# Performance work log

Measured on AMD Instinct MI355X. Metric: run time of the kernel, lower is better.

The kernel has to match this reference:

```python
import jax, jax.numpy as jnp
import numpy as np

N_NODES = 50000
N_HYPEREDGES = 50000
E = 320000
D = 256


def _prelu(x, a):
    return jnp.where(x >= 0, x, a * x)


def _hypergraph_conv(x, hei, W, b, num_nodes, num_edges):
    # PyG HypergraphConv, use_attention=False, heads=1:
    # out = D^{-1} H B^{-1} H^T (X W^T) + b
    src = hei[0]  # node indices, [E]
    he = hei[1]   # hyperedge indices, [E]
    xw = x @ W.T  # [N, D] node transform (lin has no bias)
    ones = jnp.ones((hei.shape[1],), x.dtype)
    deg_n = jax.ops.segment_sum(ones, src, num_segments=num_nodes)   # node degree D
    deg_e = jax.ops.segment_sum(ones, he, num_segments=num_edges)    # hyperedge size B
    d_inv = jnp.where(deg_n > 0, 1.0 / deg_n, 0.0)
    b_inv = jnp.where(deg_e > 0, 1.0 / deg_e, 0.0)
    # node -> hyperedge aggregation, scaled by B^{-1}
    edge_feat = b_inv[:, None] * jax.ops.segment_sum(xw[src], he, num_segments=num_edges)  # [n_he, D]
    # hyperedge -> node aggregation, scaled by D^{-1}
    out = d_inv[:, None] * jax.ops.segment_sum(edge_feat[he], src, num_segments=num_nodes)  # [N, D]
    return out + b


def setup_inputs() -> dict:
    key = jax.random.key(0)
    ks = jax.random.split(key, 6)
    std = np.sqrt(2.0 / D)  # kaiming_normal
    x = jax.random.normal(ks[0], (N_NODES, D), dtype=jnp.float32)
    hyper_edge_index = jax.random.randint(ks[1], (2, E), 0, N_HYPEREDGES, dtype=jnp.int64)
    W1 = jax.random.normal(ks[2], (D, D), dtype=jnp.float32) * std
    b1 = jnp.zeros((D,), jnp.float32)
    W2 = jax.random.normal(ks[3], (D, D), dtype=jnp.float32) * std
    b2 = jnp.zeros((D,), jnp.float32)
    prelu_a = jnp.asarray(0.25, jnp.float32)
    return {"x": x, "W1": W1, "b1": b1, "W2": W2, "b2": b2,
            "prelu_a": prelu_a, "hyper_edge_index": hyper_edge_index}


def reference(x, W1, b1, W2, b2, prelu_a, hyper_edge_index):
    out = _hypergraph_conv(x, hyper_edge_index, W1, b1, N_NODES, N_HYPEREDGES)
    out = _prelu(out, prelu_a)
    out = _hypergraph_conv(out, hyper_edge_index, W2, b2, N_NODES, N_HYPEREDGES)
    out = out + x  # residual
    out = _prelu(out, prelu_a)
    return out
```

## Files before the change

### kernel.cpp

```cpp
#include <hip/hip_runtime.h>

#define NN    50000
#define NHE   50000
#define NEDGE 320000
#define DD    256

#define SB    1024
#define NBLK  ((NN + SB - 1) / SB)

typedef float f32x4 __attribute__((ext_vector_type(4)));
typedef short short8 __attribute__((ext_vector_type(8)));

static __device__ __forceinline__ unsigned short f2b(float f) {
    union { float f; unsigned u; } c; c.f = f;
    unsigned u = c.u;
    u += 0x7fffu + ((u >> 16) & 1u);
    return (unsigned short)(u >> 16);
}
static __device__ __forceinline__ float b2f_lo(unsigned v) {
    union { unsigned u; float f; } c; c.u = v << 16; return c.f;
}
static __device__ __forceinline__ float b2f_hi(unsigned v) {
    union { unsigned u; float f; } c; c.u = v & 0xffff0000u; return c.f;
}
static __device__ __forceinline__ unsigned pack2(float a, float b) {
    return (unsigned)f2b(a) | ((unsigned)f2b(b) << 16);
}

__global__ __launch_bounds__(256) void k_count(const int* __restrict__ src,
                                               const int* __restrict__ he,
                                               int* __restrict__ cnt_n,
                                               int* __restrict__ cnt_e) {
    int e = blockIdx.x * 256 + threadIdx.x;
    if (e >= NEDGE) return;
    atomicAdd(&cnt_n[src[e]], 1);
    atomicAdd(&cnt_e[he[e]], 1);
}

__global__ __launch_bounds__(256) void k_scan_a(const int* __restrict__ cnt_n,
                                                const int* __restrict__ cnt_e,
                                                int* __restrict__ bsum) {
    int b   = blockIdx.x;
    int seg = b / NBLK, lb = b % NBLK;
    const int* cnt = seg ? cnt_e : cnt_n;
    int t = threadIdx.x;
    int idx = lb * SB + t * 4;
    int s = 0;
#pragma unroll
    for (int j = 0; j < 4; ++j)
        if (idx + j < NN) s += cnt[idx + j];
    __shared__ int red[256];
    red[t] = s;
    __syncthreads();
    for (int o = 128; o > 0; o >>= 1) {
        if (t < o) red[t] += red[t + o];
        __syncthreads();
    }
    if (t == 0) bsum[b] = red[0];
}

__global__ __launch_bounds__(64) void k_scan_b(const int* __restrict__ bsum,
                                               int* __restrict__ bbase) {
    if (threadIdx.x == 0) {
        int r = 0;
        for (int i = 0; i < NBLK; ++i) { bbase[i] = r; r += bsum[i]; }
        bbase[2 * NBLK] = r;
        r = 0;
        for (int i = NBLK; i < 2 * NBLK; ++i) { bbase[i] = r; r += bsum[i]; }
        bbase[2 * NBLK + 1] = r;
    }
}

__global__ __launch_bounds__(256) void k_scan_c(const int* __restrict__ cnt_n,
                                                const int* __restrict__ cnt_e,
                                                const int* __restrict__ bbase,
                                                int* __restrict__ off_n,
                                                int* __restrict__ off_e) {
    int b   = blockIdx.x;
    int seg = b / NBLK, lb = b % NBLK;
    const int* cnt = seg ? cnt_e : cnt_n;
    int* off = seg ? off_e : off_n;
    int t = threadIdx.x;
    int idx = lb * SB + t * 4;
    int v[4];
    int tsum = 0;
#pragma unroll
    for (int j = 0; j < 4; ++j) {
        v[j] = (idx + j < NN) ? cnt[idx + j] : 0;
        tsum += v[j];
    }
    __shared__ int sc[256];
    sc[t] = tsum;
    __syncthreads();
    for (int o = 1; o < 256; o <<= 1) {
        int val = (t >= o) ? sc[t - o] : 0;
        __syncthreads();
        sc[t] += val;
        __syncthreads();
    }
    int p = bbase[b] + sc[t] - tsum;
#pragma unroll
    for (int j = 0; j < 4; ++j) {
        if (idx + j < NN) off[idx + j] = p;
        p += v[j];
    }
    if (b == 0 && t == 0) off_n[NN] = bbase[2 * NBLK];
    if (b == NBLK && t == 0) off_e[NHE] = bbase[2 * NBLK + 1];
}

__global__ __launch_bounds__(256) void k_fill(const int* __restrict__ src,
                                              const int* __restrict__ he,
                                              const int* __restrict__ off_n,
                                              const int* __restrict__ off_e,
                                              int* __restrict__ cur_n,
                                              int* __restrict__ cur_e,
                                              int* __restrict__ adj_n,
                                              int* __restrict__ adj_e) {
    int e = blockIdx.x * 256 + threadIdx.x;
    if (e >= NEDGE) return;
    int s = src[e], h = he[e];
    int pn = off_n[s] + atomicAdd(&cur_n[s], 1);
    adj_n[pn] = h;
    int pe = off_e[h] + atomicAdd(&cur_e[h], 1);
    adj_e[pe] = s;
}

__global__ __launch_bounds__(256) void k_cvt_w(const float* __restrict__ w1,
                                               const float* __restrict__ w2,
                                               unsigned short* __restrict__ o1,
                                               unsigned short* __restrict__ o2) {
    int t = blockIdx.x * 256 + threadIdx.x;
    const int n4 = DD * DD / 4;
    const float* s = (t < n4) ? w1 : w2;
    unsigned short* d = (t < n4) ? o1 : o2;
    int i = (t < n4) ? t : t - n4;
    float4 v = ((const float4*)s)[i];
    uint2 o;
    o.x = pack2(v.x, v.y);
    o.y = pack2(v.z, v.w);
    ((uint2*)d)[i] = o;
}

template <bool A32>
__global__ __launch_bounds__(256) void k_gemm_bf16(const void* __restrict__ Av,
                                                   const unsigned short* __restrict__ Wb,
                                                   unsigned short* __restrict__ Cb, int M) {
    __shared__ __align__(16) unsigned short As[64 * 32];
    __shared__ __align__(16) unsigned short Bs[128 * 32];
    const int t    = threadIdx.x;
    const int m0   = blockIdx.x * 64;
    const int n0   = blockIdx.y * 128;
    const int lane = t & 63;
    const int wave = t >> 6;
    const int wm   = (wave >> 1) * 32;
    const int wn   = (wave & 1) * 64;
    const int fr   = lane & 15;
    const int fq   = lane >> 4;

    f32x4 acc[2][4] = {};

    const int sr = t >> 2;
    const int ss = t & 3;

    for (int k0 = 0; k0 < DD; k0 += 32) {
        uint4 av = make_uint4(0u, 0u, 0u, 0u);
        {
            int gm = m0 + sr;
            if (gm < M) {
                if (A32) {
                    const float* p = (const float*)Av + (size_t)gm * DD + k0 + ss * 8;
                    float4 f0 = *(const float4*)p;
                    float4 f1 = *(const float4*)(p + 4);
                    av.x = pack2(f0.x, f0.y);
                    av.y = pack2(f0.z, f0.w);
                    av.z = pack2(f1.x, f1.y);
                    av.w = pack2(f1.z, f1.w);
                } else {
                    av = *(const uint4*)((const unsigned short*)Av + (size_t)gm * DD + k0 + ss * 8);
                }
            }
        }
        uint4 bv0 = *(const uint4*)(Wb + (size_t)(n0 + sr) * DD + k0 + ss * 8);
        uint4 bv1 = *(const uint4*)(Wb + (size_t)(n0 + sr + 64) * DD + k0 + ss * 8);
        __syncthreads();
        *(uint4*)(As + sr * 32 + ((ss ^ (sr & 3)) * 8)) = av;
        {
            int r0 = sr, r1 = sr + 64;
            *(uint4*)(Bs + r0 * 32 + ((ss ^ (r0 & 3)) * 8)) = bv0;
            *(uint4*)(Bs + r1 * 32 + ((ss ^ (r1 & 3)) * 8)) = bv1;
        }
        __syncthreads();

        short8 af[2], bf[4];
#pragma unroll
        for (int mt = 0; mt < 2; ++mt) {
            int r = wm + mt * 16 + fr;
            af[mt] = *(const short8*)(As + r * 32 + ((fq ^ (r & 3)) * 8));
        }
#pragma unroll
        for (int nt = 0; nt < 4; ++nt) {
            int r = wn + nt * 16 + fr;
            bf[nt] = *(const short8*)(Bs + r * 32 + ((fq ^ (r & 3)) * 8));
        }
#pragma unroll
        for (int mt = 0; mt < 2; ++mt)
#pragma unroll
            for (int nt = 0; nt < 4; ++nt)
                acc[mt][nt] = __builtin_amdgcn_mfma_f32_16x16x32_bf16(af[mt], bf[nt],
                                                                      acc[mt][nt], 0, 0, 0);
    }

#pragma unroll
    for (int mt = 0; mt < 2; ++mt) {
#pragma unroll
        for (int i = 0; i < 4; ++i) {
            int gm = m0 + wm + mt * 16 + fq * 4 + i;
            if (gm >= M) continue;
#pragma unroll
            for (int nt = 0; nt < 4; ++nt) {
                int gn = n0 + wn + nt * 16 + fr;
                Cb[(size_t)gm * DD + gn] = f2b(acc[mt][nt][i]);
            }
        }
    }
}

static __device__ __forceinline__ void acc8(float* a, uint4 v) {
    a[0] += b2f_lo(v.x); a[1] += b2f_hi(v.x);
    a[2] += b2f_lo(v.y); a[3] += b2f_hi(v.y);
    a[4] += b2f_lo(v.z); a[5] += b2f_hi(v.z);
    a[6] += b2f_lo(v.w); a[7] += b2f_hi(v.w);
}
static __device__ __forceinline__ void gather8(const unsigned short* __restrict__ srcb,
                                               const int* __restrict__ adj,
                                               int b, int e, int sl, float* a) {
#pragma unroll
    for (int i = 0; i < 8; ++i) a[i] = 0.f;
    for (int i = b; i < e; i += 8) {
        int g0 = adj[i];
        int g[8];
        g[0] = g0;
#pragma unroll
        for (int j = 1; j < 8; ++j) g[j] = (i + j < e) ? adj[i + j] : g0;
        uint4 v[8];
#pragma unroll
        for (int j = 0; j < 8; ++j)
            v[j] = *(const uint4*)(srcb + (size_t)g[j] * DD + sl * 8);
        acc8(a, v[0]);
#pragma unroll
        for (int j = 1; j < 8; ++j)
            if (i + j < e) acc8(a, v[j]);
    }
}

__global__ __launch_bounds__(256) void k_gather_edge_b(const unsigned short* __restrict__ xw,
                                                       unsigned short* __restrict__ ef,
                                                       const int* __restrict__ off,
                                                       const int* __restrict__ adj) {
    int tid = blockIdx.x * 256 + threadIdx.x;
    int w = tid >> 5;
    int sl = tid & 31;
    if (w >= NHE) return;
    int b = off[w], e = off[w + 1];
    float a[8];
    gather8(xw, adj, b, e, sl, a);
    float sc = (e > b) ? 1.f / (float)(e - b) : 0.f;
    uint4 o;
    o.x = pack2(a[0] * sc, a[1] * sc);
    o.y = pack2(a[2] * sc, a[3] * sc);
    o.z = pack2(a[4] * sc, a[5] * sc);
    o.w = pack2(a[6] * sc, a[7] * sc);
    *(uint4*)(ef + (size_t)w * DD + sl * 8) = o;
}

__global__ __launch_bounds__(256) void k_gather_node_mid_b(const unsigned short* __restrict__ ef,
                                                           unsigned short* __restrict__ h,
                                                           const int* __restrict__ off,
                                                           const int* __restrict__ adj,
                                                           const float* __restrict__ bias,
                                                           const float* __restrict__ aP) {
    int tid = blockIdx.x * 256 + threadIdx.x;
    int w = tid >> 5;
    int sl = tid & 31;
    if (w >= NN) return;
    int b = off[w], e = off[w + 1];
    float a[8];
    gather8(ef, adj, b, e, sl, a);
    float sc = (e > b) ? 1.f / (float)(e - b) : 0.f;
    float al = *aP;
    float4 bb0 = ((const float4*)bias)[sl * 2];
    float4 bb1 = ((const float4*)bias)[sl * 2 + 1];
    float r[8];
    r[0] = a[0] * sc + bb0.x; r[1] = a[1] * sc + bb0.y;
    r[2] = a[2] * sc + bb0.z; r[3] = a[3] * sc + bb0.w;
    r[4] = a[4] * sc + bb1.x; r[5] = a[5] * sc + bb1.y;
    r[6] = a[6] * sc + bb1.z; r[7] = a[7] * sc + bb1.w;
#pragma unroll
    for (int i = 0; i < 8; ++i) r[i] = (r[i] >= 0.f) ? r[i] : al * r[i];
    uint4 o;
    o.x = pack2(r[0], r[1]);
    o.y = pack2(r[2], r[3]);
    o.z = pack2(r[4], r[5]);
    o.w = pack2(r[6], r[7]);
    *(uint4*)(h + (size_t)w * DD + sl * 8) = o;
}

__global__ __launch_bounds__(256) void k_gather_node_final_b(const unsigned short* __restrict__ ef,
                                                             const float* __restrict__ x,
                                                             float* __restrict__ out,
                                                             const int* __restrict__ off,
                                                             const int* __restrict__ adj,
                                                             const float* __restrict__ bias,
                                                             const float* __restrict__ aP) {
    int tid = blockIdx.x * 256 + threadIdx.x;
    int w = tid >> 5;
    int sl = tid & 31;
    if (w >= NN) return;
    int b = off[w], e = off[w + 1];
    float a[8];
    gather8(ef, adj, b, e, sl, a);
    float sc = (e > b) ? 1.f / (float)(e - b) : 0.f;
    float al = *aP;
    float4 bb0 = ((const float4*)bias)[sl * 2];
    float4 bb1 = ((const float4*)bias)[sl * 2 + 1];
    const float* xp = x + (size_t)w * DD + sl * 8;
    float4 xv0 = *(const float4*)xp;
    float4 xv1 = *(const float4*)(xp + 4);
    float r[8];
    r[0] = a[0] * sc + bb0.x + xv0.x; r[1] = a[1] * sc + bb0.y + xv0.y;
    r[2] = a[2] * sc + bb0.z + xv0.z; r[3] = a[3] * sc + bb0.w + xv0.w;
    r[4] = a[4] * sc + bb1.x + xv1.x; r[5] = a[5] * sc + bb1.y + xv1.y;
    r[6] = a[6] * sc + bb1.z + xv1.z; r[7] = a[7] * sc + bb1.w + xv1.w;
#pragma unroll
    for (int i = 0; i < 8; ++i) r[i] = (r[i] >= 0.f) ? r[i] : al * r[i];
    float* op = out + (size_t)w * DD + sl * 8;
    *(float4*)op = make_float4(r[0], r[1], r[2], r[3]);
    *(float4*)(op + 4) = make_float4(r[4], r[5], r[6], r[7]);
}

extern "C" void kernel_launch(void* const* d_in, const int* in_sizes, int n_in,
                              void* d_out, int out_size, void* d_ws, size_t ws_size,
                              hipStream_t stream) {
    const float* x       = (const float*)d_in[0];
    const float* W1      = (const float*)d_in[1];
    const float* b1      = (const float*)d_in[2];
    const float* W2      = (const float*)d_in[3];
    const float* b2      = (const float*)d_in[4];
    const float* prelu_a = (const float*)d_in[5];
    const int*   hei     = (const int*)d_in[6];
    const int* idx_src = hei;
    const int* idx_he  = hei + NEDGE;

    float* out = (float*)d_out;
    unsigned short* B1 = (unsigned short*)d_ws;
    unsigned short* B2 = B1 + (size_t)NN * DD;
    int* off_n = (int*)(B2 + (size_t)NN * DD);
    int* off_e = off_n + NN + 1;
    int* cur_n = off_e + NHE + 1;
    int* cur_e = cur_n + NN;
    int* adj_n = cur_e + NHE;
    int* adj_e = adj_n + NEDGE;
    int* bsum  = adj_e + NEDGE;
    int* bbase = bsum + 2 * NBLK;
    unsigned short* w1b = (unsigned short*)d_out;
    unsigned short* w2b = w1b + DD * DD;

    const int eblocks = (NEDGE + 255) / 256;
    const int gblocks = (NN * 32 + 255) / 256;
    dim3 ggrid((NN + 63) / 64, DD / 128);

    hipMemsetAsync(cur_n, 0, sizeof(int) * (NN + NHE), stream);
    k_count<<<eblocks, 256, 0, stream>>>(idx_src, idx_he, cur_n, cur_e);
    k_scan_a<<<2 * NBLK, 256, 0, stream>>>(cur_n, cur_e, bsum);
    k_scan_b<<<1, 64, 0, stream>>>(bsum, bbase);
    k_scan_c<<<2 * NBLK, 256, 0, stream>>>(cur_n, cur_e, bbase, off_n, off_e);
    hipMemsetAsync(cur_n, 0, sizeof(int) * (NN + NHE), stream);
    k_fill<<<eblocks, 256, 0, stream>>>(idx_src, idx_he, off_n, off_e,
                                        cur_n, cur_e, adj_n, adj_e);

    k_cvt_w<<<(2 * DD * DD / 4 + 255) / 256, 256, 0, stream>>>(W1, W2, w1b, w2b);

    k_gemm_bf16<true><<<ggrid, 256, 0, stream>>>((const void*)x, w1b, B1, NN);
    k_gather_edge_b<<<gblocks, 256, 0, stream>>>(B1, B2, off_e, adj_e);
    k_gather_node_mid_b<<<gblocks, 256, 0, stream>>>(B2, B1, off_n, adj_n, b1, prelu_a);

    k_gemm_bf16<false><<<ggrid, 256, 0, stream>>>((const void*)B1, w2b, B2, NN);
    k_gather_edge_b<<<gblocks, 256, 0, stream>>>(B2, B1, off_e, adj_e);
    k_gather_node_final_b<<<gblocks, 256, 0, stream>>>(B1, x, out, off_n, adj_n, b2, prelu_a);
}
```

Baseline: 332.8 us.

## Fuse CSR build and weight conversion into one cooperative kernel; stage GEMM stores

Replaces the two memsets and six small launches (count, three scan stages, fill, weight conversion) with a single cooperative kernel that uses grid-wide syncs between phases and resets the counters during the scan. This is meant to cut launch and inter-kernel gap overhead on the preprocessing path. Separately, the GEMM swaps its grid axes and writes its bf16 output through shared memory so it can issue coalesced 16-byte stores instead of scattered 2-byte stores. The cost is grid-sync latency inside a 98-block cooperative launch and some extra LDS traffic and barriers in the GEMM epilogue.

```diff
diff --git a/kernel.cpp b/kernel.cpp
--- a/kernel.cpp
+++ b/kernel.cpp
@@ -1,4 +1,7 @@
 #include <hip/hip_runtime.h>
+#include <hip/hip_cooperative_groups.h>
+
+namespace cg = cooperative_groups;
 
 #define NN    50000
 #define NHE   50000
@@ -27,41 +30,63 @@
     return (unsigned)f2b(a) | ((unsigned)f2b(b) << 16);
 }
 
-__global__ __launch_bounds__(256) void k_count(const int* __restrict__ src,
-                                               const int* __restrict__ he,
-                                               int* __restrict__ cnt_n,
-                                               int* __restrict__ cnt_e) {
-    int e = blockIdx.x * 256 + threadIdx.x;
-    if (e >= NEDGE) return;
-    atomicAdd(&cnt_n[src[e]], 1);
-    atomicAdd(&cnt_e[he[e]], 1);
-}
-
-__global__ __launch_bounds__(256) void k_scan_a(const int* __restrict__ cnt_n,
-                                                const int* __restrict__ cnt_e,
-                                                int* __restrict__ bsum) {
-    int b   = blockIdx.x;
-    int seg = b / NBLK, lb = b % NBLK;
-    const int* cnt = seg ? cnt_e : cnt_n;
-    int t = threadIdx.x;
-    int idx = lb * SB + t * 4;
-    int s = 0;
-#pragma unroll
-    for (int j = 0; j < 4; ++j)
-        if (idx + j < NN) s += cnt[idx + j];
+__global__ __launch_bounds__(256) void k_csr(const int* __restrict__ src,
+                                             const int* __restrict__ he,
+                                             int* __restrict__ cnt_n,
+                                             int* __restrict__ cnt_e,
+                                             int* __restrict__ off_n,
+                                             int* __restrict__ off_e,
+                                             int* __restrict__ adj_n,
+                                             int* __restrict__ adj_e,
+                                             int* __restrict__ bsum,
+                                             int* __restrict__ bbase,
+                                             const float* __restrict__ w1,
+                                             const float* __restrict__ w2,
+                                             unsigned short* __restrict__ o1,
+                                             unsigned short* __restrict__ o2) {
+    cg::grid_group g = cg::this_grid();
+    const int tid  = blockIdx.x * 256 + threadIdx.x;
+    const int nthr = gridDim.x * 256;
     __shared__ int red[256];
-    red[t] = s;
-    __syncthreads();
-    for (int o = 128; o > 0; o >>= 1) {
-        if (t < o) red[t] += red[t + o];
-        __syncthreads();
-    }
-    if (t == 0) bsum[b] = red[0];
-}
-
-__global__ __launch_bounds__(64) void k_scan_b(const int* __restrict__ bsum,
-                                               int* __restrict__ bbase) {
-    if (threadIdx.x == 0) {
+
+    for (int i = tid; i < NN + NHE; i += nthr) cnt_n[i] = 0;
+    const int n4 = DD * DD / 4;
+    for (int i = tid; i < 2 * n4; i += nthr) {
+        const float* s = (i < n4) ? w1 : w2;
+        unsigned short* d = (i < n4) ? o1 : o2;
+        int j = (i < n4) ? i : i - n4;
+        float4 v = ((const float4*)s)[j];
+        uint2 o; o.x = pack2(v.x, v.y); o.y = pack2(v.z, v.w);
+        ((uint2*)d)[j] = o;
+    }
+    g.sync();
+
+    for (int e = tid; e < NEDGE; e += nthr) {
+        atomicAdd(&cnt_n[src[e]], 1);
+        atomicAdd(&cnt_e[he[e]], 1);
+    }
+    g.sync();
+
+    {
+        int b = blockIdx.x, seg = b / NBLK, lb = b % NBLK;
+        const int* cnt = seg ? cnt_e : cnt_n;
+        int t = threadIdx.x;
+        int idx = lb * SB + t * 4;
+        int s = 0;
+#pragma unroll
+        for (int j = 0; j < 4; ++j)
+            if (idx + j < NN) s += cnt[idx + j];
+        red[t] = s;
+        __syncthreads();
+        for (int o = 128; o > 0; o >>= 1) {
+            if (t < o) red[t] += red[t + o];
+            __syncthreads();
+        }
+        if (t == 0) bsum[b] = red[0];
+    }
+    g.sync();
+
+    if (tid == 0) {
         int r = 0;
         for (int i = 0; i < NBLK; ++i) { bbase[i] = r; r += bsum[i]; }
         bbase[2 * NBLK] = r;
@@ -69,87 +94,60 @@
         for (int i = NBLK; i < 2 * NBLK; ++i) { bbase[i] = r; r += bsum[i]; }
         bbase[2 * NBLK + 1] = r;
     }
-}
-
-__global__ __launch_bounds__(256) void k_scan_c(const int* __restrict__ cnt_n,
-                                                const int* __restrict__ cnt_e,
-                                                const int* __restrict__ bbase,
-                                                int* __restrict__ off_n,
-                                                int* __restrict__ off_e) {
-    int b   = blockIdx.x;
-    int seg = b / NBLK, lb = b % NBLK;
-    const int* cnt = seg ? cnt_e : cnt_n;
-    int* off = seg ? off_e : off_n;
-    int t = threadIdx.x;
-    int idx = lb * SB + t * 4;
-    int v[4];
-    int tsum = 0;
-#pragma unroll
-    for (int j = 0; j < 4; ++j) {
-        v[j] = (idx + j < NN) ? cnt[idx + j] : 0;
-        tsum += v[j];
-    }
-    __shared__ int sc[256];
-    sc[t] = tsum;
-    __syncthreads();
-    for (int o = 1; o < 256; o <<= 1) {
-        int val = (t >= o) ? sc[t - o] : 0;
-        __syncthreads();
-        sc[t] += val;
-        __syncthreads();
-    }
-    int p = bbase[b] + sc[t] - tsum;
-#pragma unroll
-    for (int j = 0; j < 4; ++j) {
-        if (idx + j < NN) off[idx + j] = p;
-        p += v[j];
-    }
-    if (b == 0 && t == 0) off_n[NN] = bbase[2 * NBLK];
-    if (b == NBLK && t == 0) off_e[NHE] = bbase[2 * NBLK + 1];
-}
-
-__global__ __launch_bounds__(256) void k_fill(const int* __restrict__ src,
-                                              const int* __restrict__ he,
-                                              const int* __restrict__ off_n,
-                                              const int* __restrict__ off_e,
-                                              int* __restrict__ cur_n,
-                                              int* __restrict__ cur_e,
-                                              int* __restrict__ adj_n,
-                                              int* __restrict__ adj_e) {
-    int e = blockIdx.x * 256 + threadIdx.x;
-    if (e >= NEDGE) return;
-    int s = src[e], h = he[e];
-    int pn = off_n[s] + atomicAdd(&cur_n[s], 1);
-    adj_n[pn] = h;
-    int pe = off_e[h] + atomicAdd(&cur_e[h], 1);
-    adj_e[pe] = s;
-}
-
-__global__ __launch_bounds__(256) void k_cvt_w(const float* __restrict__ w1,
-                                               const float* __restrict__ w2,
-                                               unsigned short* __restrict__ o1,
-                                               unsigned short* __restrict__ o2) {
-    int t = blockIdx.x * 256 + threadIdx.x;
-    const int n4 = DD * DD / 4;
-    const float* s = (t < n4) ? w1 : w2;
-    unsigned short* d = (t < n4) ? o1 : o2;
-    int i = (t < n4) ? t : t - n4;
-    float4 v = ((const float4*)s)[i];
-    uint2 o;
-    o.x = pack2(v.x, v.y);
-    o.y = pack2(v.z, v.w);
-    ((uint2*)d)[i] = o;
+    g.sync();
+
+    {
+        int b = blockIdx.x, seg = b / NBLK, lb = b % NBLK;
+        int* cnt = seg ? cnt_e : cnt_n;
+        int* off = seg ? off_e : off_n;
+        int t = threadIdx.x;
+        int idx = lb * SB + t * 4;
+        int v[4];
+        int tsum = 0;
+#pragma unroll
+        for (int j = 0; j < 4; ++j) {
+            v[j] = (idx + j < NN) ? cnt[idx + j] : 0;
+            tsum += v[j];
+        }
+        __syncthreads();
+        red[t] = tsum;
+        __syncthreads();
+        for (int o = 1; o < 256; o <<= 1) {
+            int val = (t >= o) ? red[t - o] : 0;
+            __syncthreads();
+            red[t] += val;
+            __syncthreads();
+        }
+        int p = bbase[b] + red[t] - tsum;
+#pragma unroll
+        for (int j = 0; j < 4; ++j) {
+            if (idx + j < NN) { off[idx + j] = p; cnt[idx + j] = 0; }
+            p += v[j];
+        }
+        if (b == 0 && t == 0) off_n[NN] = bbase[2 * NBLK];
+        if (b == NBLK && t == 0) off_e[NHE] = bbase[2 * NBLK + 1];
+    }
+    g.sync();
+
+    for (int e = tid; e < NEDGE; e += nthr) {
+        int s = src[e], h = he[e];
+        int pn = off_n[s] + atomicAdd(&cnt_n[s], 1);
+        adj_n[pn] = h;
+        int pe = off_e[h] + atomicAdd(&cnt_e[h], 1);
+        adj_e[pe] = s;
+    }
 }
 
 template <bool A32>
 __global__ __launch_bounds__(256) void k_gemm_bf16(const void* __restrict__ Av,
                                                    const unsigned short* __restrict__ Wb,
                                                    unsigned short* __restrict__ Cb, int M) {
-    __shared__ __align__(16) unsigned short As[64 * 32];
-    __shared__ __align__(16) unsigned short Bs[128 * 32];
+    __shared__ __align__(16) unsigned short sh[64 * 32 + 128 * 32];
+    unsigned short* As = sh;
+    unsigned short* Bs = sh + 64 * 32;
     const int t    = threadIdx.x;
-    const int m0   = blockIdx.x * 64;
-    const int n0   = blockIdx.y * 128;
+    const int m0   = blockIdx.y * 64;
+    const int n0   = blockIdx.x * 128;
     const int lane = t & 63;
     const int wave = t >> 6;
     const int wm   = (wave >> 1) * 32;
@@ -210,16 +208,26 @@
                                                                       acc[mt][nt], 0, 0, 0);
     }
 
+    const int SW = 72;
+    unsigned short* Sw = sh + wave * (16 * SW);
 #pragma unroll
     for (int mt = 0; mt < 2; ++mt) {
-#pragma unroll
-        for (int i = 0; i < 4; ++i) {
-            int gm = m0 + wm + mt * 16 + fq * 4 + i;
-            if (gm >= M) continue;
-#pragma unroll
-            for (int nt = 0; nt < 4; ++nt) {
-                int gn = n0 + wn + nt * 16 + fr;
-                Cb[(size_t)gm * DD + gn] = f2b(acc[mt][nt][i]);
+        __syncthreads();
+#pragma unroll
+        for (int i = 0; i < 4; ++i)
+#pragma unroll
+            for (int nt = 0; nt < 4; ++nt)
+                Sw[(fq * 4 + i) * SW + nt * 16 + fr] = f2b(acc[mt][nt][i]);
+        __syncthreads();
+        int r0 = lane >> 3;
+        int c0 = (lane & 7) * 8;
+#pragma unroll
+        for (int p = 0; p < 2; ++p) {
+            int r = r0 + p * 8;
+            int gm = m0 + wm + mt * 16 + r;
+            if (gm < M) {
+                uint4 v = *(const uint4*)(Sw + r * SW + c0);
+                *(uint4*)(Cb + (size_t)gm * DD + n0 + wn + c0) = v;
             }
         }
     }
@@ -365,20 +373,15 @@
     unsigned short* w1b = (unsigned short*)d_out;
     unsigned short* w2b = w1b + DD * DD;
 
-    const int eblocks = (NEDGE + 255) / 256;
     const int gblocks = (NN * 32 + 255) / 256;
-    dim3 ggrid((NN + 63) / 64, DD / 128);
-
-    hipMemsetAsync(cur_n, 0, sizeof(int) * (NN + NHE), stream);
-    k_count<<<eblocks, 256, 0, stream>>>(idx_src, idx_he, cur_n, cur_e);
-    k_scan_a<<<2 * NBLK, 256, 0, stream>>>(cur_n, cur_e, bsum);
-    k_scan_b<<<1, 64, 0, stream>>>(bsum, bbase);
-    k_scan_c<<<2 * NBLK, 256, 0, stream>>>(cur_n, cur_e, bbase, off_n, off_e);
-    hipMemsetAsync(cur_n, 0, sizeof(int) * (NN + NHE), stream);
-    k_fill<<<eblocks, 256, 0, stream>>>(idx_src, idx_he, off_n, off_e,
-                                        cur_n, cur_e, adj_n, adj_e);
-
-    k_cvt_w<<<(2 * DD * DD / 4 + 255) / 256, 256, 0, stream>>>(W1, W2, w1b, w2b);
+    dim3 ggrid(DD / 128, (NN + 63) / 64);
+
+    void* cargs[] = {(void*)&idx_src, (void*)&idx_he, (void*)&cur_n, (void*)&cur_e,
+                     (void*)&off_n, (void*)&off_e, (void*)&adj_n, (void*)&adj_e,
+                     (void*)&bsum, (void*)&bbase, (void*)&W1, (void*)&W2,
+                     (void*)&w1b, (void*)&w2b};
+    hipLaunchCooperativeKernel((const void*)k_csr, dim3(2 * NBLK), dim3(256),
+                               cargs, 0, stream);
 
     k_gemm_bf16<true><<<ggrid, 256, 0, stream>>>((const void*)x, w1b, B1, NN);
     k_gather_edge_b<<<gblocks, 256, 0, stream>>>(B1, B2, off_e, adj_e);
```

Result: slower. 402.2 us (+20.9%).
